# Kernel optimization log

Hardware: AMD Instinct MI355X
Metric: run time of the kernel (lower is better)

## Reference

```python
import jax, jax.numpy as jnp
import numpy as np

N_NODES = 100000
N_EDGES = 1000000
N_GRAPHS = 256
NUM_NODE_TYPES = 200
EMB_DIM = 64
HID_DIM = 32


def _gcn_conv(x, src, dst, W, b, n):
    """PyG GCNConv: x' = D^-1/2 (A+I) D^-1/2 (x W) + b. src/dst already include self-loops."""
    xw = x @ W  # [n, out]
    ones = jnp.ones(dst.shape, dtype=xw.dtype)
    deg = jax.ops.segment_sum(ones, dst, num_segments=n)  # in-degree incl. self-loop
    dinv = jnp.where(deg > 0, jax.lax.rsqrt(jnp.maximum(deg, 1e-12)), 0.0)
    norm = dinv[src] * dinv[dst]  # [E+n]
    msg = xw[src] * norm[:, None]  # gather + scale
    return jax.ops.segment_sum(msg, dst, num_segments=n) + b


def setup_inputs() -> dict:
    key = jax.random.key(0)
    ks = jax.random.split(key, 12)
    x = jax.random.randint(ks[0], (N_NODES, 1), 0, NUM_NODE_TYPES, dtype=jnp.int64)
    edge_index = jax.random.randint(ks[1], (2, N_EDGES), 0, N_NODES, dtype=jnp.int64)
    batch = jnp.sort(jax.random.randint(ks[2], (N_NODES,), 0, N_GRAPHS, dtype=jnp.int64))
    s = 0.05
    emb = jax.random.normal(ks[3], (NUM_NODE_TYPES, EMB_DIM), dtype=jnp.float32)
    W1 = jax.random.normal(ks[4], (EMB_DIM, HID_DIM), dtype=jnp.float32) * s
    b1 = jnp.zeros((HID_DIM,), dtype=jnp.float32)
    W2 = jax.random.normal(ks[5], (HID_DIM, HID_DIM), dtype=jnp.float32) * s
    b2 = jnp.zeros((HID_DIM,), dtype=jnp.float32)
    Wc1 = jax.random.normal(ks[6], (HID_DIM, 16), dtype=jnp.float32) * s
    bc1 = jnp.zeros((16,), dtype=jnp.float32)
    Wc2 = jax.random.normal(ks[7], (16, 1), dtype=jnp.float32) * s
    bc2 = jnp.zeros((1,), dtype=jnp.float32)
    return dict(x=x, edge_index=edge_index, batch=batch, emb=emb, W1=W1, b1=b1,
                W2=W2, b2=b2, Wc1=Wc1, bc1=bc1, Wc2=Wc2, bc2=bc2)


def reference(x, edge_index, batch, emb, W1, b1, W2, b2, Wc1, bc1, Wc2, bc2):
    n = x.shape[0]
    ids = x[:, 0]  # x.squeeze()
    loops = jnp.arange(n, dtype=edge_index.dtype)
    src = jnp.concatenate([edge_index[0], loops])
    dst = jnp.concatenate([edge_index[1], loops])

    h = emb[ids]  # [N, 64] embedding lookup
    h = jax.nn.relu(_gcn_conv(h, src, dst, W1, b1, n))
    h = jax.nn.relu(_gcn_conv(h, src, dst, W2, b2, n))

    # global_mean_pool over batch segments
    seg_sum = jax.ops.segment_sum(h, batch, num_segments=N_GRAPHS)
    counts = jax.ops.segment_sum(jnp.ones((n,), dtype=h.dtype), batch, num_segments=N_GRAPHS)
    pooled = seg_sum / jnp.maximum(counts, 1.0)[:, None]  # [B, 32]

    hc = jax.nn.relu(pooled @ Wc1 + bc1)
    return jax.nn.sigmoid(hc @ Wc2 + bc2)  # [B, 1]
```

## Files before the change

kernel.cpp:

```cpp
#include <hip/hip_runtime.h>
#include <hip/hip_fp16.h>
#include <math.h>

#define N_NODES   100000
#define N_EDGES   1000000
#define N_GRAPHS  256
#define NUM_TYPES 200
#define EMB       64
#define HID       32
#define BSHIFT    8
#define BSTRIDE   256
#define NBUCK     391
#define EPB       4096
#define NCHUNK    245
#define MAXBE     4096
#define SRCBITS   17
#define SRCMASK   0x1FFFF
#define ELOC      1024


__global__ __launch_bounds__(256) void k_binA(const int* __restrict__ dst,
                                              int* __restrict__ counts) {
    __shared__ int cnt[NBUCK];
    int tid = threadIdx.x, k = blockIdx.x;
    for (int b = tid; b < NBUCK; b += 256) cnt[b] = 0;
    __syncthreads();
    int base = k * EPB;
    int n = min(EPB, N_EDGES - base);
    for (int t = tid; t < n; t += 256) atomicAdd(&cnt[dst[base + t] >> BSHIFT], 1);
    __syncthreads();
    for (int b = tid; b < NBUCK; b += 256) counts[k * NBUCK + b] = cnt[b];
}

__global__ __launch_bounds__(512) void k_misc(const int* __restrict__ counts,
                                              int* __restrict__ offs,
                                              int* __restrict__ bbase,
                                              const float* __restrict__ emb,
                                              const float* __restrict__ W1,
                                              float* __restrict__ table,
                                              float* __restrict__ pooled) {
    int tid = threadIdx.x;
    if (blockIdx.x == 0) {
        __shared__ int sA[512], sB[512];
        int total = 0;
        if (tid < NBUCK)
            for (int k = 0; k < NCHUNK; ++k) total += counts[k * NBUCK + tid];
        sA[tid] = (tid < NBUCK) ? total : 0;
        __syncthreads();
        int* in = sA; int* ot = sB;
        for (int off = 1; off < 512; off <<= 1) {
            ot[tid] = in[tid] + (tid >= off ? in[tid - off] : 0);
            __syncthreads();
            int* tmp = in; in = ot; ot = tmp;
        }
        int excl = in[tid] - ((tid < NBUCK) ? total : 0);
        if (tid < NBUCK) {
            bbase[tid] = excl;
            int run = excl;
            for (int k = 0; k < NCHUNK; ++k) {
                offs[k * NBUCK + tid] = run;
                run += counts[k * NBUCK + tid];
            }
        }
        if (tid == 0) bbase[NBUCK] = N_EDGES;
    } else if (blockIdx.x == 1) {
        for (int t = tid; t < NUM_TYPES * HID; t += 512) {
            int ty = t / HID, j = t % HID;
            float s = 0.f;
            for (int k = 0; k < EMB; ++k) s = fmaf(emb[ty * EMB + k], W1[k * HID + j], s);
            table[t] = s;
        }
    } else {
        for (int t = tid; t < N_GRAPHS * HID; t += 512) pooled[t] = 0.f;
    }
}

__global__ __launch_bounds__(512) void k_binB(const int* __restrict__ src,
                                              const int* __restrict__ dst,
                                              const int* __restrict__ offs,
                                              int* __restrict__ binned) {
    __shared__ int srcl[EPB];
    __shared__ int dstl[EPB];
    __shared__ unsigned short rank16[EPB];
    __shared__ unsigned short perm[EPB];
    __shared__ int cnt[NBUCK];
    __shared__ int loc[NBUCK];
    __shared__ int offsL[NBUCK];
    __shared__ int sA[512], sB[512];
    int tid = threadIdx.x, k = blockIdx.x;
    int base = k * EPB;
    int n = min(EPB, N_EDGES - base);
    if (tid < NBUCK) { cnt[tid] = 0; offsL[tid] = offs[k * NBUCK + tid]; }
    __syncthreads();
    for (int t = tid; t < n; t += 512) {
        int s = src[base + t], d = dst[base + t];
        srcl[t] = s; dstl[t] = d;
        rank16[t] = (unsigned short)atomicAdd(&cnt[d >> BSHIFT], 1);
    }
    __syncthreads();
    sA[tid] = (tid < NBUCK) ? cnt[tid] : 0;
    __syncthreads();
    int* in = sA; int* ot = sB;
    for (int off = 1; off < 512; off <<= 1) {
        ot[tid] = in[tid] + (tid >= off ? in[tid - off] : 0);
        __syncthreads();
        int* tmp = in; in = ot; ot = tmp;
    }
    if (tid < NBUCK) loc[tid] = in[tid] - cnt[tid];
    __syncthreads();
    for (int t = tid; t < n; t += 512) {
        int b = dstl[t] >> BSHIFT;
        perm[loc[b] + rank16[t]] = (unsigned short)t;
    }
    __syncthreads();
    for (int t = tid; t < n; t += 512) {
        int e = perm[t];
        int d = dstl[e], b = d >> BSHIFT;
        int gpos = offsL[b] + (t - loc[b]);
        binned[gpos] = ((d & (BSTRIDE - 1)) << SRCBITS) | srcl[e];
    }
}

__global__ __launch_bounds__(512) void k_csr(const int* __restrict__ binned,
                                             const int* __restrict__ bbase,
                                             const int* __restrict__ ids,
                                             int* __restrict__ ssrc,
                                             int* __restrict__ row_ptr,
                                             float* __restrict__ dinv,
                                             int2* __restrict__ nodeinfo) {
    __shared__ int pk[MAXBE];
    __shared__ unsigned char dl[MAXBE];
    __shared__ unsigned short rank16[MAXBE];
    __shared__ unsigned short perm[MAXBE];
    __shared__ int degL[BSTRIDE];
    __shared__ int loc[BSTRIDE];
    __shared__ int sA[BSTRIDE], sB[BSTRIDE];
    int tid = threadIdx.x, b = blockIdx.x;
    int e0 = bbase[b], e1 = bbase[b + 1];
    int n = min(e1 - e0, MAXBE);
    if (tid < BSTRIDE) degL[tid] = 0;
    __syncthreads();
    for (int t = tid; t < n; t += 512) {
        int v = binned[e0 + t];
        pk[t] = v;
        int d = v >> SRCBITS;
        dl[t] = (unsigned char)d;
        rank16[t] = (unsigned short)atomicAdd(&degL[d], 1);
    }
    __syncthreads();
    if (tid < BSTRIDE) sA[tid] = degL[tid];
    __syncthreads();
    int* in = sA; int* ot = sB;
    for (int off = 1; off < BSTRIDE; off <<= 1) {
        if (tid < BSTRIDE) ot[tid] = in[tid] + (tid >= off ? in[tid - off] : 0);
        __syncthreads();
        int* tmp = in; in = ot; ot = tmp;
    }
    if (tid < BSTRIDE) loc[tid] = in[tid] - degL[tid];
    __syncthreads();
    for (int t = tid; t < n; t += 512)
        perm[loc[dl[t]] + rank16[t]] = (unsigned short)t;
    __syncthreads();
    for (int t = tid; t < n; t += 512)
        ssrc[e0 + t] = pk[perm[t]] & SRCMASK;
    if (tid < BSTRIDE) {
        int i = b * BSTRIDE + tid;
        if (i < N_NODES) {
            row_ptr[i] = e0 + loc[tid];
            float dv = rsqrtf((float)degL[tid] + 1.0f);
            dinv[i] = dv;
            nodeinfo[i] = make_int2(ids[i], __float_as_int(dv));
        }
    }
    if (b == NBUCK - 1 && tid == 0) row_ptr[N_NODES] = N_EDGES;
}


__global__ __launch_bounds__(256) void k_gather1(
        const int2* __restrict__ nodeinfo, const float* __restrict__ table,
        const int* __restrict__ row_ptr, const int* __restrict__ ssrc,
        const float* __restrict__ b1, const float* __restrict__ W2,
        uint2* __restrict__ Y2h) {
    __shared__ float w[HID * HID];
    __shared__ unsigned int eloc[ELOC];
    int tid = threadIdx.x;
    for (int k = tid; k < HID * HID; k += 256) w[k] = W2[k];

    int i0 = (blockIdx.x * 256) >> 3;
    int eb0 = row_ptr[i0];
    int eb1 = row_ptr[i0 + 32];
    int ne = eb1 - eb0;
    bool fits = (ne <= ELOC);
    if (fits) {
        for (int t = tid; t < ne; t += 256) {
            int s = ssrc[eb0 + t];
            int2 ni = nodeinfo[s];
            eloc[t] = ((unsigned)ni.x << 16) |
                      __half_as_ushort(__float2half(__int_as_float(ni.y)));
        }
    }
    __syncthreads();

    int t = blockIdx.x * 256 + tid;
    int i = t >> 3, p = t & 7;
    const float4* tab4 = (const float4*)table;

    int s0 = row_ptr[i], n = row_ptr[i + 1] - s0;
    int l0 = s0 - eb0;
    int2 self = nodeinfo[i];
    float di = __int_as_float(self.y);
    float4 acc = tab4[self.x * 8 + p];
    acc.x *= di; acc.y *= di; acc.z *= di; acc.w *= di;

    if (fits) {
        for (int e = 0; e < n; e += 8) {
            unsigned int ei[8];
#pragma unroll
            for (int u = 0; u < 8; ++u) {
                int idx = e + u; idx = (idx > n - 1) ? n - 1 : idx;
                ei[u] = eloc[l0 + idx];
            }
#pragma unroll
            for (int u = 0; u < 8; ++u) {
                float ds = (e + u < n)
                    ? __half2float(__ushort_as_half((unsigned short)(ei[u] & 0xFFFF))) : 0.f;
                float4 v = tab4[(ei[u] >> 16) * 8 + p];
                acc.x = fmaf(v.x, ds, acc.x);
                acc.y = fmaf(v.y, ds, acc.y);
                acc.z = fmaf(v.z, ds, acc.z);
                acc.w = fmaf(v.w, ds, acc.w);
            }
        }
    } else {
        for (int e = 0; e < n; ++e) {
            int s = ssrc[s0 + e];
            int2 ni = nodeinfo[s];
            float ds = __half2float(__float2half(__int_as_float(ni.y)));
            float4 v = tab4[ni.x * 8 + p];
            acc.x = fmaf(v.x, ds, acc.x);
            acc.y = fmaf(v.y, ds, acc.y);
            acc.z = fmaf(v.z, ds, acc.z);
            acc.w = fmaf(v.w, ds, acc.w);
        }
    }
    float4 bb = ((const float4*)b1)[p];
    float4 h;
    h.x = fmaxf(fmaf(di, acc.x, bb.x), 0.f);
    h.y = fmaxf(fmaf(di, acc.y, bb.y), 0.f);
    h.z = fmaxf(fmaf(di, acc.z, bb.z), 0.f);
    h.w = fmaxf(fmaf(di, acc.w, bb.w), 0.f);

    float o0 = 0.f, o1 = 0.f, o2 = 0.f, o3 = 0.f;
    const float4* w4 = (const float4*)w;
#pragma unroll
    for (int q = 0; q < 8; ++q) {
        float4 hq;
        hq.x = __shfl(h.x, q, 8);
        hq.y = __shfl(h.y, q, 8);
        hq.z = __shfl(h.z, q, 8);
        hq.w = __shfl(h.w, q, 8);
        float4 w0 = w4[(4 * q + 0) * 8 + p];
        float4 w1 = w4[(4 * q + 1) * 8 + p];
        float4 w2 = w4[(4 * q + 2) * 8 + p];
        float4 w3 = w4[(4 * q + 3) * 8 + p];
        o0 = fmaf(hq.x, w0.x, o0); o1 = fmaf(hq.x, w0.y, o1); o2 = fmaf(hq.x, w0.z, o2); o3 = fmaf(hq.x, w0.w, o3);
        o0 = fmaf(hq.y, w1.x, o0); o1 = fmaf(hq.y, w1.y, o1); o2 = fmaf(hq.y, w1.z, o2); o3 = fmaf(hq.y, w1.w, o3);
        o0 = fmaf(hq.z, w2.x, o0); o1 = fmaf(hq.z, w2.y, o1); o2 = fmaf(hq.z, w2.z, o2); o3 = fmaf(hq.z, w2.w, o3);
        o0 = fmaf(hq.w, w3.x, o0); o1 = fmaf(hq.w, w3.y, o1); o2 = fmaf(hq.w, w3.z, o2); o3 = fmaf(hq.w, w3.w, o3);
    }
    __half2 h01 = __halves2half2(__float2half(o0 * di), __float2half(o1 * di));
    __half2 h23 = __halves2half2(__float2half(o2 * di), __float2half(o3 * di));
    uint2 wv;
    wv.x = *(unsigned int*)&h01;
    wv.y = *(unsigned int*)&h23;
    Y2h[i * 8 + p] = wv;
}

__global__ __launch_bounds__(256) void k_gather2(
        const uint2* __restrict__ Y2h, const int* __restrict__ row_ptr,
        const int* __restrict__ ssrc, const float* __restrict__ dinv,
        const float* __restrict__ b2, const int* __restrict__ batch,
        float* __restrict__ pooled) {
    __shared__ float lp[32][HID];
    for (int k = threadIdx.x; k < 32 * HID; k += 256) ((float*)lp)[k] = 0.f;
    __syncthreads();

    int t = blockIdx.x * 256 + threadIdx.x;
    int i = t >> 3, p = t & 7;
    int i0 = (blockIdx.x * 256) >> 3;
    int gFirst = batch[i0];

    uint2 selfv = Y2h[i * 8 + p];
    float2 sa = __half22float2(*(__half2*)&selfv.x);
    float2 sb = __half22float2(*(__half2*)&selfv.y);
    float4 acc = make_float4(sa.x, sa.y, sb.x, sb.y);

    int s0 = row_ptr[i], n = row_ptr[i + 1] - s0;
    for (int e = 0; e < n; e += 8) {
        int ss[8];
#pragma unroll
        for (int u = 0; u < 8; ++u) {
            int idx = e + u; idx = (idx > n - 1) ? n - 1 : idx;
            ss[u] = ssrc[s0 + idx];
        }
        uint2 v[8];
#pragma unroll
        for (int u = 0; u < 8; ++u) v[u] = Y2h[ss[u] * 8 + p];
#pragma unroll
        for (int u = 0; u < 8; ++u) {
            float wg = (e + u < n) ? 1.f : 0.f;
            float2 fa = __half22float2(*(__half2*)&v[u].x);
            float2 fb = __half22float2(*(__half2*)&v[u].y);
            acc.x = fmaf(fa.x, wg, acc.x);
            acc.y = fmaf(fa.y, wg, acc.y);
            acc.z = fmaf(fb.x, wg, acc.z);
            acc.w = fmaf(fb.y, wg, acc.w);
        }
    }
    float di = dinv[i];
    float4 bb = ((const float4*)b2)[p];
    float4 h;
    h.x = fmaxf(fmaf(di, acc.x, bb.x), 0.f);
    h.y = fmaxf(fmaf(di, acc.y, bb.y), 0.f);
    h.z = fmaxf(fmaf(di, acc.z, bb.z), 0.f);
    h.w = fmaxf(fmaf(di, acc.w, bb.w), 0.f);

    int gl = batch[i] - gFirst;
    atomicAdd(&lp[gl][p * 4 + 0], h.x);
    atomicAdd(&lp[gl][p * 4 + 1], h.y);
    atomicAdd(&lp[gl][p * 4 + 2], h.z);
    atomicAdd(&lp[gl][p * 4 + 3], h.w);
    __syncthreads();

    int gLast = batch[i0 + 31];
    int ng = gLast - gFirst + 1;
    for (int k = threadIdx.x; k < ng * HID; k += 256) {
        float v = lp[k / HID][k % HID];
        if (v != 0.f) atomicAdd(&pooled[(gFirst + k / HID) * HID + (k % HID)], v);
    }
}

__global__ void k_head(const float* __restrict__ pooled, const int* __restrict__ batch,
                       const float* __restrict__ Wc1, const float* __restrict__ bc1,
                       const float* __restrict__ Wc2, const float* __restrict__ bc2,
                       float* __restrict__ out) {
    int g = blockIdx.x * blockDim.x + threadIdx.x;
    if (g >= N_GRAPHS) return;
    int lo = 0, hi = N_NODES;
    while (lo < hi) { int mid = (lo + hi) >> 1; if (batch[mid] < g) lo = mid + 1; else hi = mid; }
    int start = lo;
    hi = N_NODES;
    while (lo < hi) { int mid = (lo + hi) >> 1; if (batch[mid] < g + 1) lo = mid + 1; else hi = mid; }
    int end = lo;
    float inv = 1.0f / fmaxf((float)(end - start), 1.0f);
    float m[HID];
    for (int j = 0; j < HID; ++j) m[j] = pooled[g * HID + j] * inv;
    float hc[16];
    for (int j = 0; j < 16; ++j) {
        float s = bc1[j];
        for (int k = 0; k < HID; ++k) s = fmaf(m[k], Wc1[k * 16 + j], s);
        hc[j] = fmaxf(s, 0.f);
    }
    float s = bc2[0];
    for (int k = 0; k < 16; ++k) s = fmaf(hc[k], Wc2[k], s);
    out[g] = 1.0f / (1.0f + expf(-s));
}


extern "C" void kernel_launch(void* const* d_in, const int* in_sizes, int n_in,
                              void* d_out, int out_size, void* d_ws, size_t ws_size,
                              hipStream_t stream) {
    const int*   ids  = (const int*)d_in[0];
    const int*   src  = (const int*)d_in[1];
    const int*   dst  = ((const int*)d_in[1]) + N_EDGES;
    const int*   batch = (const int*)d_in[2];
    const float* emb  = (const float*)d_in[3];
    const float* W1   = (const float*)d_in[4];
    const float* b1   = (const float*)d_in[5];
    const float* W2   = (const float*)d_in[6];
    const float* b2   = (const float*)d_in[7];
    const float* Wc1  = (const float*)d_in[8];
    const float* bc1  = (const float*)d_in[9];
    const float* Wc2  = (const float*)d_in[10];
    const float* bc2  = (const float*)d_in[11];
    float* out = (float*)d_out;

    int* W = (int*)d_ws;
    size_t o = 0;
    uint2* Y2h      = (uint2*)(W + o);        o += 1600000;
    int*   binned   = W + o;                  o += N_EDGES;
    int*   ssrc     = W + o;                  o += N_EDGES;
    int2*  nodeinfo = (int2*)(W + o);         o += 2 * N_NODES;
    int*   counts   = W + o;                  o += NCHUNK * NBUCK;
    int*   offs     = W + o;                  o += NCHUNK * NBUCK;
    int*   bbase    = W + o;                  o += NBUCK + 1;
    int*   row_ptr  = W + o;                  o += N_NODES + 1;
    o = (o + 3) & ~(size_t)3;
    float* dinv     = (float*)(W + o);        o += N_NODES;
    float* table    = (float*)(W + o);        o += NUM_TYPES * HID;
    float* pooled   = (float*)(W + o);

    const int B = 256;
    const int gNode8 = (N_NODES * 8) / B;

    k_binA<<<NCHUNK, B, 0, stream>>>(dst, counts);
    k_misc<<<3, 512, 0, stream>>>(counts, offs, bbase, emb, W1, table, pooled);
    k_binB<<<NCHUNK, 512, 0, stream>>>(src, dst, offs, binned);
    k_csr<<<NBUCK, 512, 0, stream>>>(binned, bbase, ids, ssrc, row_ptr, dinv, nodeinfo);

    k_gather1<<<gNode8, B, 0, stream>>>(nodeinfo, table, row_ptr, ssrc, b1, W2, Y2h);
    k_gather2<<<gNode8, B, 0, stream>>>((const uint2*)Y2h, row_ptr, ssrc, dinv, b2,
                                        batch, pooled);
    k_head<<<1, N_GRAPHS, 0, stream>>>(pooled, batch, Wc1, bc1, Wc2, bc2, out);
}
```

Before: 117.9 us.

## Replace global bucket count/scan with chunk-local sort and per-bucket gather in CSR

Drops the separate counting pass and the global scan kernel. Each chunk now sorts its edges by bucket locally, writes them in place and records per-bucket counts and offsets. The CSR kernel then scans those per-chunk counts itself and copies its bucket's slices from every chunk into shared memory. Row pointers and the dinv array are replaced by a packed per-node int4 (start, degree, type id, dinv), and ssrc uses a fixed MAXBE stride per bucket. This removes two launches and one pass over dst. In exchange the CSR kernel does a serial, scattered per-chunk copy, and any bucket with more than MAXBE edges would be silently truncated.

```diff
diff --git a/kernel.cpp b/kernel.cpp
--- a/kernel.cpp
+++ b/kernel.cpp
@@ -19,78 +19,39 @@
 #define ELOC      1024
 
 
-__global__ __launch_bounds__(256) void k_binA(const int* __restrict__ dst,
-                                              int* __restrict__ counts) {
-    __shared__ int cnt[NBUCK];
-    int tid = threadIdx.x, k = blockIdx.x;
-    for (int b = tid; b < NBUCK; b += 256) cnt[b] = 0;
-    __syncthreads();
-    int base = k * EPB;
-    int n = min(EPB, N_EDGES - base);
-    for (int t = tid; t < n; t += 256) atomicAdd(&cnt[dst[base + t] >> BSHIFT], 1);
-    __syncthreads();
-    for (int b = tid; b < NBUCK; b += 256) counts[k * NBUCK + b] = cnt[b];
-}
-
-__global__ __launch_bounds__(512) void k_misc(const int* __restrict__ counts,
-                                              int* __restrict__ offs,
-                                              int* __restrict__ bbase,
-                                              const float* __restrict__ emb,
-                                              const float* __restrict__ W1,
-                                              float* __restrict__ table,
-                                              float* __restrict__ pooled) {
-    int tid = threadIdx.x;
-    if (blockIdx.x == 0) {
-        __shared__ int sA[512], sB[512];
-        int total = 0;
-        if (tid < NBUCK)
-            for (int k = 0; k < NCHUNK; ++k) total += counts[k * NBUCK + tid];
-        sA[tid] = (tid < NBUCK) ? total : 0;
-        __syncthreads();
-        int* in = sA; int* ot = sB;
-        for (int off = 1; off < 512; off <<= 1) {
-            ot[tid] = in[tid] + (tid >= off ? in[tid - off] : 0);
-            __syncthreads();
-            int* tmp = in; in = ot; ot = tmp;
-        }
-        int excl = in[tid] - ((tid < NBUCK) ? total : 0);
-        if (tid < NBUCK) {
-            bbase[tid] = excl;
-            int run = excl;
-            for (int k = 0; k < NCHUNK; ++k) {
-                offs[k * NBUCK + tid] = run;
-                run += counts[k * NBUCK + tid];
-            }
-        }
-        if (tid == 0) bbase[NBUCK] = N_EDGES;
-    } else if (blockIdx.x == 1) {
+__global__ __launch_bounds__(512) void k_bin(const int* __restrict__ src,
+                                             const int* __restrict__ dst,
+                                             int* __restrict__ binned,
+                                             int* __restrict__ counts,
+                                             int* __restrict__ locg,
+                                             const float* __restrict__ emb,
+                                             const float* __restrict__ W1,
+                                             float* __restrict__ table,
+                                             float* __restrict__ pooled) {
+    int tid = threadIdx.x, c = blockIdx.x;
+    if (c == NCHUNK) {
         for (int t = tid; t < NUM_TYPES * HID; t += 512) {
             int ty = t / HID, j = t % HID;
             float s = 0.f;
             for (int k = 0; k < EMB; ++k) s = fmaf(emb[ty * EMB + k], W1[k * HID + j], s);
             table[t] = s;
         }
-    } else {
+        return;
+    }
+    if (c == NCHUNK + 1) {
         for (int t = tid; t < N_GRAPHS * HID; t += 512) pooled[t] = 0.f;
-    }
-}
-
-__global__ __launch_bounds__(512) void k_binB(const int* __restrict__ src,
-                                              const int* __restrict__ dst,
-                                              const int* __restrict__ offs,
-                                              int* __restrict__ binned) {
+        return;
+    }
     __shared__ int srcl[EPB];
     __shared__ int dstl[EPB];
     __shared__ unsigned short rank16[EPB];
     __shared__ unsigned short perm[EPB];
     __shared__ int cnt[NBUCK];
     __shared__ int loc[NBUCK];
-    __shared__ int offsL[NBUCK];
     __shared__ int sA[512], sB[512];
-    int tid = threadIdx.x, k = blockIdx.x;
-    int base = k * EPB;
+    int base = c * EPB;
     int n = min(EPB, N_EDGES - base);
-    if (tid < NBUCK) { cnt[tid] = 0; offsL[tid] = offs[k * NBUCK + tid]; }
+    if (tid < NBUCK) cnt[tid] = 0;
     __syncthreads();
     for (int t = tid; t < n; t += 512) {
         int s = src[base + t], d = dst[base + t];
@@ -115,42 +76,68 @@
     __syncthreads();
     for (int t = tid; t < n; t += 512) {
         int e = perm[t];
-        int d = dstl[e], b = d >> BSHIFT;
-        int gpos = offsL[b] + (t - loc[b]);
-        binned[gpos] = ((d & (BSTRIDE - 1)) << SRCBITS) | srcl[e];
-    }
-}
+        binned[base + t] = ((dstl[e] & (BSTRIDE - 1)) << SRCBITS) | srcl[e];
+    }
+    if (tid < NBUCK) {
+        counts[c * NBUCK + tid] = cnt[tid];
+        locg[c * NBUCK + tid] = loc[tid];
+    }
+}
+
 
 __global__ __launch_bounds__(512) void k_csr(const int* __restrict__ binned,
-                                             const int* __restrict__ bbase,
+                                             const int* __restrict__ counts,
+                                             const int* __restrict__ locg,
                                              const int* __restrict__ ids,
                                              int* __restrict__ ssrc,
-                                             int* __restrict__ row_ptr,
-                                             float* __restrict__ dinv,
-                                             int2* __restrict__ nodeinfo) {
+                                             int2* __restrict__ nodeinfo,
+                                             int4* __restrict__ nmeta) {
     __shared__ int pk[MAXBE];
     __shared__ unsigned char dl[MAXBE];
     __shared__ unsigned short rank16[MAXBE];
     __shared__ unsigned short perm[MAXBE];
     __shared__ int degL[BSTRIDE];
     __shared__ int loc[BSTRIDE];
-    __shared__ int sA[BSTRIDE], sB[BSTRIDE];
+    __shared__ int sA[512], sB[512];
+    __shared__ int ccnt[NCHUNK];
+    __shared__ int cloc[NCHUNK];
+    __shared__ int cbase[NCHUNK];
     int tid = threadIdx.x, b = blockIdx.x;
-    int e0 = bbase[b], e1 = bbase[b + 1];
-    int n = min(e1 - e0, MAXBE);
+
+    if (tid < NCHUNK) {
+        ccnt[tid] = counts[tid * NBUCK + b];
+        cloc[tid] = locg[tid * NBUCK + b];
+    }
+    __syncthreads();
+    sA[tid] = (tid < NCHUNK) ? ccnt[tid] : 0;
+    __syncthreads();
+    int* in = sA; int* ot = sB;
+    for (int off = 1; off < 512; off <<= 1) {
+        ot[tid] = in[tid] + (tid >= off ? in[tid - off] : 0);
+        __syncthreads();
+        int* tmp = in; in = ot; ot = tmp;
+    }
+    if (tid < NCHUNK) cbase[tid] = in[tid] - ccnt[tid];
+    __syncthreads();
+    int n = min(in[NCHUNK - 1], MAXBE);
+    for (int c = tid; c < NCHUNK; c += 512) {
+        int m = ccnt[c];
+        int gsrc = c * EPB + cloc[c];
+        int ldst = cbase[c];
+        for (int j = 0; j < m; ++j) pk[ldst + j] = binned[gsrc + j];
+    }
     if (tid < BSTRIDE) degL[tid] = 0;
     __syncthreads();
+
     for (int t = tid; t < n; t += 512) {
-        int v = binned[e0 + t];
-        pk[t] = v;
-        int d = v >> SRCBITS;
+        int d = pk[t] >> SRCBITS;
         dl[t] = (unsigned char)d;
         rank16[t] = (unsigned short)atomicAdd(&degL[d], 1);
     }
     __syncthreads();
     if (tid < BSTRIDE) sA[tid] = degL[tid];
     __syncthreads();
-    int* in = sA; int* ot = sB;
+    in = sA; ot = sB;
     for (int off = 1; off < BSTRIDE; off <<= 1) {
         if (tid < BSTRIDE) ot[tid] = in[tid] + (tid >= off ? in[tid - off] : 0);
         __syncthreads();
@@ -161,24 +148,23 @@
     for (int t = tid; t < n; t += 512)
         perm[loc[dl[t]] + rank16[t]] = (unsigned short)t;
     __syncthreads();
+    int e0 = b * MAXBE;
     for (int t = tid; t < n; t += 512)
         ssrc[e0 + t] = pk[perm[t]] & SRCMASK;
     if (tid < BSTRIDE) {
         int i = b * BSTRIDE + tid;
         if (i < N_NODES) {
-            row_ptr[i] = e0 + loc[tid];
             float dv = rsqrtf((float)degL[tid] + 1.0f);
-            dinv[i] = dv;
             nodeinfo[i] = make_int2(ids[i], __float_as_int(dv));
-        }
-    }
-    if (b == NBUCK - 1 && tid == 0) row_ptr[N_NODES] = N_EDGES;
+            nmeta[i] = make_int4(e0 + loc[tid], degL[tid], ids[i], __float_as_int(dv));
+        }
+    }
 }
 
 
 __global__ __launch_bounds__(256) void k_gather1(
-        const int2* __restrict__ nodeinfo, const float* __restrict__ table,
-        const int* __restrict__ row_ptr, const int* __restrict__ ssrc,
+        const int2* __restrict__ nodeinfo, const int4* __restrict__ nmeta,
+        const float* __restrict__ table, const int* __restrict__ ssrc,
         const float* __restrict__ b1, const float* __restrict__ W2,
         uint2* __restrict__ Y2h) {
     __shared__ float w[HID * HID];
@@ -187,9 +173,10 @@
     for (int k = tid; k < HID * HID; k += 256) w[k] = W2[k];
 
     int i0 = (blockIdx.x * 256) >> 3;
-    int eb0 = row_ptr[i0];
-    int eb1 = row_ptr[i0 + 32];
-    int ne = eb1 - eb0;
+    int4 m0 = nmeta[i0];
+    int4 m31 = nmeta[i0 + 31];
+    int eb0 = m0.x;
+    int ne = m31.x + m31.y - eb0;
     bool fits = (ne <= ELOC);
     if (fits) {
         for (int t = tid; t < ne; t += 256) {
@@ -205,11 +192,11 @@
     int i = t >> 3, p = t & 7;
     const float4* tab4 = (const float4*)table;
 
-    int s0 = row_ptr[i], n = row_ptr[i + 1] - s0;
+    int4 nm = nmeta[i];
+    int s0 = nm.x, n = nm.y;
     int l0 = s0 - eb0;
-    int2 self = nodeinfo[i];
-    float di = __int_as_float(self.y);
-    float4 acc = tab4[self.x * 8 + p];
+    float di = __int_as_float(nm.w);
+    float4 acc = tab4[nm.z * 8 + p];
     acc.x *= di; acc.y *= di; acc.z *= di; acc.w *= di;
 
     if (fits) {
@@ -277,10 +264,9 @@
 }
 
 __global__ __launch_bounds__(256) void k_gather2(
-        const uint2* __restrict__ Y2h, const int* __restrict__ row_ptr,
-        const int* __restrict__ ssrc, const float* __restrict__ dinv,
-        const float* __restrict__ b2, const int* __restrict__ batch,
-        float* __restrict__ pooled) {
+        const uint2* __restrict__ Y2h, const int4* __restrict__ nmeta,
+        const int* __restrict__ ssrc, const float* __restrict__ b2,
+        const int* __restrict__ batch, float* __restrict__ pooled) {
     __shared__ float lp[32][HID];
     for (int k = threadIdx.x; k < 32 * HID; k += 256) ((float*)lp)[k] = 0.f;
     __syncthreads();
@@ -295,7 +281,8 @@
     float2 sb = __half22float2(*(__half2*)&selfv.y);
     float4 acc = make_float4(sa.x, sa.y, sb.x, sb.y);
 
-    int s0 = row_ptr[i], n = row_ptr[i + 1] - s0;
+    int4 nm = nmeta[i];
+    int s0 = nm.x, n = nm.y;
     for (int e = 0; e < n; e += 8) {
         int ss[8];
 #pragma unroll
@@ -317,7 +304,7 @@
             acc.w = fmaf(fb.y, wg, acc.w);
         }
     }
-    float di = dinv[i];
+    float di = __int_as_float(nm.w);
     float4 bb = ((const float4*)b2)[p];
     float4 h;
     h.x = fmaxf(fmaf(di, acc.x, bb.x), 0.f);
@@ -389,27 +376,24 @@
     size_t o = 0;
     uint2* Y2h      = (uint2*)(W + o);        o += 1600000;
     int*   binned   = W + o;                  o += N_EDGES;
-    int*   ssrc     = W + o;                  o += N_EDGES;
+    int*   ssrc     = W + o;                  o += NBUCK * MAXBE;
     int2*  nodeinfo = (int2*)(W + o);         o += 2 * N_NODES;
-    int*   counts   = W + o;                  o += NCHUNK * NBUCK;
-    int*   offs     = W + o;                  o += NCHUNK * NBUCK;
-    int*   bbase    = W + o;                  o += NBUCK + 1;
-    int*   row_ptr  = W + o;                  o += N_NODES + 1;
+    int4*  nmeta    = (int4*)(W + o);         o += 4 * N_NODES;
+    int*   counts   = W + o;                  o += NCHUNK * NBUCK + 1;
     o = (o + 3) & ~(size_t)3;
-    float* dinv     = (float*)(W + o);        o += N_NODES;
+    int*   locg     = W + o;                  o += NCHUNK * NBUCK;
+    o = (o + 3) & ~(size_t)3;
     float* table    = (float*)(W + o);        o += NUM_TYPES * HID;
     float* pooled   = (float*)(W + o);
 
     const int B = 256;
     const int gNode8 = (N_NODES * 8) / B;
 
-    k_binA<<<NCHUNK, B, 0, stream>>>(dst, counts);
-    k_misc<<<3, 512, 0, stream>>>(counts, offs, bbase, emb, W1, table, pooled);
-    k_binB<<<NCHUNK, 512, 0, stream>>>(src, dst, offs, binned);
-    k_csr<<<NBUCK, 512, 0, stream>>>(binned, bbase, ids, ssrc, row_ptr, dinv, nodeinfo);
-
-    k_gather1<<<gNode8, B, 0, stream>>>(nodeinfo, table, row_ptr, ssrc, b1, W2, Y2h);
-    k_gather2<<<gNode8, B, 0, stream>>>((const uint2*)Y2h, row_ptr, ssrc, dinv, b2,
-                                        batch, pooled);
+    k_bin<<<NCHUNK + 2, 512, 0, stream>>>(src, dst, binned, counts, locg,
+                                          emb, W1, table, pooled);
+    k_csr<<<NBUCK, 512, 0, stream>>>(binned, counts, locg, ids, ssrc, nodeinfo, nmeta);
+
+    k_gather1<<<gNode8, B, 0, stream>>>(nodeinfo, nmeta, table, ssrc, b1, W2, Y2h);
+    k_gather2<<<gNode8, B, 0, stream>>>((const uint2*)Y2h, nmeta, ssrc, b2, batch, pooled);
     k_head<<<1, N_GRAPHS, 0, stream>>>(pooled, batch, Wc1, bc1, Wc2, bc2, out);
 }
```

Result: faster. 104.0 us (-11.8%).
